# Optimization experiments

Hardware: AMD Instinct MI355X
Metric: run time of the kernel (lower is better)

## Reference

```python
import jax, jax.numpy as jnp
import numpy as np

DIM = 192
HRES, WRES = 64, 64
NUM_HEADS = 6
WS = 8  # window_size
MLP_HIDDEN = int(DIM * 4.0)
EPS = 1e-5


def layer_norm(x, gamma, beta):
    mu = jnp.mean(x, axis=-1, keepdims=True)
    var = jnp.var(x, axis=-1, keepdims=True)
    return (x - mu) * jax.lax.rsqrt(var + EPS) * gamma + beta


def window_partition(x, ws):
    B, H, W, C = x.shape
    x = x.reshape(B, H // ws, ws, W // ws, ws, C)
    x = jnp.transpose(x, (0, 1, 3, 2, 4, 5))
    return x.reshape(-1, ws * ws, C)


def window_reverse(windows, ws, H, W, C):
    B = windows.shape[0] // ((H // ws) * (W // ws))
    x = windows.reshape(B, H // ws, W // ws, ws, ws, C)
    x = jnp.transpose(x, (0, 1, 3, 2, 4, 5))
    return x.reshape(B, H, W, C)


def setup_inputs() -> dict:
    key = jax.random.key(0)
    ks = jax.random.split(key, 12)
    s = 0.02
    return {
        "x": jax.random.normal(ks[0], (32, HRES * WRES, DIM), dtype=jnp.float32),
        "norm1_g": jnp.ones((DIM,), jnp.float32),
        "norm1_b": jnp.zeros((DIM,), jnp.float32),
        "qkv_w": jax.random.normal(ks[1], (DIM, 3 * DIM), jnp.float32) * s,
        "qkv_b": jnp.zeros((3 * DIM,), jnp.float32),
        "proj_w": jax.random.normal(ks[2], (DIM, DIM), jnp.float32) * s,
        "proj_b": jnp.zeros((DIM,), jnp.float32),
        "norm2_g": jnp.ones((DIM,), jnp.float32),
        "norm2_b": jnp.zeros((DIM,), jnp.float32),
        "fc1_w": jax.random.normal(ks[3], (DIM, MLP_HIDDEN), jnp.float32) * s,
        "fc1_b": jnp.zeros((MLP_HIDDEN,), jnp.float32),
        "fc2_w": jax.random.normal(ks[4], (MLP_HIDDEN, DIM), jnp.float32) * s,
        "fc2_b": jnp.zeros((DIM,), jnp.float32),
    }


def reference(x, norm1_g, norm1_b, qkv_w, qkv_b, proj_w, proj_b,
              norm2_g, norm2_b, fc1_w, fc1_b, fc2_w, fc2_b):
    B, L, C = x.shape
    H, W = HRES, WRES
    hd = C // NUM_HEADS
    scale = hd ** -0.5

    shortcut = x
    h = layer_norm(x, norm1_g, norm1_b).reshape(B, H, W, C)
    win = window_partition(h, WS)  # [nW*B, WS*WS, C]
    Bw, N, _ = win.shape

    qkv = (win @ qkv_w + qkv_b).reshape(Bw, N, 3, NUM_HEADS, hd)
    q, k, v = jnp.transpose(qkv, (2, 0, 3, 1, 4))  # each [Bw, H, N, hd]
    attn = jnp.einsum('bhnd,bhmd->bhnm', q, k) * scale
    attn = jax.nn.softmax(attn, axis=-1)
    out = jnp.einsum('bhnm,bhmd->bhnd', attn, v)
    out = jnp.transpose(out, (0, 2, 1, 3)).reshape(Bw, N, C)
    out = out @ proj_w + proj_b

    h = window_reverse(out, WS, H, W, C).reshape(B, L, C)
    x = shortcut + h

    m = layer_norm(x, norm2_g, norm2_b)
    m = jax.nn.gelu(m @ fc1_w + fc1_b, approximate=False)
    m = m @ fc2_w + fc2_b
    return x + m
```

## Files before the change

kernel.cpp:

```cpp
#include <hip/hip_runtime.h>
#include <hip/hip_bf16.h>
#include <math.h>

#define DIM   192
#define NH    6
#define HD    32
#define WSZ   8
#define HRES_ 64
#define WRES_ 64
#define BATCH 32
#define LTOK  (HRES_*WRES_)
#define MTOK  (BATCH*LTOK)
#define QKVN  (3*DIM)
#define MLPH  (4*DIM)

using bf16 = __hip_bfloat16;
using bf16x8 = __attribute__((ext_vector_type(8))) short;
using f32x4  = __attribute__((ext_vector_type(4))) float;

__device__ __forceinline__ float bf2f(bf16 h) { return __bfloat162float(h); }
__device__ __forceinline__ float us2f(unsigned short u) {
    union { unsigned u32; float f; } c; c.u32 = ((unsigned)u) << 16; return c.f;
}


__global__ void detect_kernel(const unsigned short* __restrict__ g, int* __restrict__ flag)
{
    *flag = (g[0] == 0x3F80) ? 0 : 1;
}

__global__ __launch_bounds__(256) void cvt_kernel(
    const void* __restrict__ src, bf16* __restrict__ dst,
    long n, long elem_off, const int* __restrict__ flag)
{
    long i = ((long)blockIdx.x * 256 + threadIdx.x) * 8;
    if (i >= n) return;
    if (i + 8 <= n) {
        if (*flag) {
            const float* s = (const float*)src + elem_off + i;
            float4 a = *reinterpret_cast<const float4*>(s);
            float4 b = *reinterpret_cast<const float4*>(s + 4);
            bf16 o[8];
            o[0]=__float2bfloat16(a.x); o[1]=__float2bfloat16(a.y);
            o[2]=__float2bfloat16(a.z); o[3]=__float2bfloat16(a.w);
            o[4]=__float2bfloat16(b.x); o[5]=__float2bfloat16(b.y);
            o[6]=__float2bfloat16(b.z); o[7]=__float2bfloat16(b.w);
            *reinterpret_cast<bf16x8*>(dst + i) = *reinterpret_cast<const bf16x8*>(o);
        } else {
            *reinterpret_cast<bf16x8*>(dst + i) =
                *reinterpret_cast<const bf16x8*>((const bf16*)src + elem_off + i);
        }
    } else {
        for (long k2 = i; k2 < n; ++k2) {
            if (*flag) dst[k2] = __float2bfloat16(((const float*)src)[elem_off + k2]);
            else       dst[k2] = ((const bf16*)src)[elem_off + k2];
        }
    }
}

__global__ __launch_bounds__(256) void ln1_fused(
    const void* __restrict__ x, long eoff, const int* __restrict__ flag,
    const bf16* __restrict__ g, const bf16* __restrict__ b, bf16* __restrict__ y)
{
    int wave = threadIdx.x >> 6;
    int lane = threadIdx.x & 63;
    long token = (long)blockIdx.x * 4 + wave;
    int fl = *flag;
    float f0, f1, f2;
    if (fl) {
        const float* xp = (const float*)x + eoff + token * DIM;
        f0 = xp[lane]; f1 = xp[lane + 64]; f2 = xp[lane + 128];
    } else {
        const bf16* xp = (const bf16*)x + eoff + token * DIM;
        f0 = bf2f(xp[lane]); f1 = bf2f(xp[lane + 64]); f2 = bf2f(xp[lane + 128]);
    }
    float s  = f0 + f1 + f2;
    float ss = f0*f0 + f1*f1 + f2*f2;
    #pragma unroll
    for (int m = 1; m < 64; m <<= 1) { s += __shfl_xor(s, m); ss += __shfl_xor(ss, m); }
    float mean = s * (1.0f/192.0f);
    float var  = ss * (1.0f/192.0f) - mean*mean;
    float rstd = rsqrtf(var + 1e-5f);
    bf16* yp = y + token * DIM;
    yp[lane]       = __float2bfloat16((f0-mean)*rstd*bf2f(g[lane])       + bf2f(b[lane]));
    yp[lane + 64]  = __float2bfloat16((f1-mean)*rstd*bf2f(g[lane + 64])  + bf2f(b[lane + 64]));
    yp[lane + 128] = __float2bfloat16((f2-mean)*rstd*bf2f(g[lane + 128]) + bf2f(b[lane + 128]));
}

__global__ void transpose_kernel(const bf16* __restrict__ in, bf16* __restrict__ out,
                                 int K, int N)
{
    int idx = blockIdx.x * 256 + threadIdx.x;
    if (idx < K * N) {
        int n = idx % N, k = idx / N;
        out[n * K + k] = in[idx];
    }
}

template<int EPI>
__global__ __launch_bounds__(256) void gemm_bt(
    const bf16* __restrict__ A, const bf16* __restrict__ Bt,
    const bf16* __restrict__ bias, const void* __restrict__ res,
    long resoff, const int* __restrict__ flag,
    bf16* __restrict__ C, int M, int N, int K)
{
    constexpr int KC = 192;
    __shared__ __align__(16) bf16 bsh[(KC/32) * 4 * 64 * 8];
    int tid  = threadIdx.x;
    int wave = tid >> 6, lane = tid & 63;
    int t = lane & 15, q = lane >> 4;
    int  n0 = blockIdx.x * 64;
    long m0 = (long)blockIdx.y * 128;

    int fl = (EPI == 2) ? *flag : 0;
    f32x4 acc[2][4] = {};

    for (int kc = 0; kc < K; kc += KC) {
        __syncthreads();
        for (int s = tid; s < (KC/32) * 256; s += 256) {
            int ks  = s >> 8;
            int rem = s & 255;
            int j   = rem >> 6;
            int ln  = rem & 63;
            int tt = ln & 15, qq = ln >> 4;
            int n = j * 16 + tt;
            int k = ks * 32 + qq * 8;
            const float4* src = reinterpret_cast<const float4*>(
                Bt + (long)(n0 + n) * K + kc + k);
            reinterpret_cast<float4*>(bsh)[s] = *src;
        }
        __syncthreads();

        const bf16* arow = A + (m0 + wave * 32 + t) * (long)K + kc + q * 8;
        #pragma unroll
        for (int ks = 0; ks < KC/32; ++ks) {
            bf16x8 a0 = *reinterpret_cast<const bf16x8*>(arow + ks * 32);
            bf16x8 a1 = *reinterpret_cast<const bf16x8*>(arow + 16 * (long)K + ks * 32);
            #pragma unroll
            for (int j = 0; j < 4; ++j) {
                bf16x8 b = reinterpret_cast<const bf16x8*>(bsh)[ks * 256 + j * 64 + lane];
                acc[0][j] = __builtin_amdgcn_mfma_f32_16x16x32_bf16(a0, b, acc[0][j], 0, 0, 0);
                acc[1][j] = __builtin_amdgcn_mfma_f32_16x16x32_bf16(a1, b, acc[1][j], 0, 0, 0);
            }
        }
    }

    #pragma unroll
    for (int j = 0; j < 4; ++j) {
        int col = n0 + j * 16 + t;
        float bv = bf2f(bias[col]);
        #pragma unroll
        for (int i = 0; i < 2; ++i) {
            #pragma unroll
            for (int r = 0; r < 4; ++r) {
                long row = m0 + wave * 32 + i * 16 + q * 4 + r;
                float v = acc[i][j][r] + bv;
                if (EPI == 2) {
                    long ri = resoff + row * (long)N + col;
                    v += fl ? ((const float*)res)[ri]
                            : bf2f(((const bf16*)res)[ri]);
                }
                C[row * N + col] = __float2bfloat16(v);
            }
        }
    }
}

__global__ __launch_bounds__(256, 3) void mlp_kernel(
    const bf16* __restrict__ Y,   const bf16* __restrict__ W1t,
    const bf16* __restrict__ b1,  const bf16* __restrict__ W2t,
    const bf16* __restrict__ b2,  const bf16* __restrict__ n2g,
    const bf16* __restrict__ n2b, const int* __restrict__ flag,
    void* __restrict__ out, long outoff, int M)
{
    constexpr int HS = 88;
    __shared__ __align__(16) bf16 bsh[1536 * 8];
    __shared__ __align__(16) bf16 hsh[64 * HS];
    int tid  = threadIdx.x;
    int wave = tid >> 6, lane = tid & 63;
    int t = lane & 15, q = lane >> 4;
    long m0 = (long)blockIdx.x * 64;
    int fl = *flag;

    bf16x8 a_reg[6];
    {
        const bf16* yp = Y + (m0 + wave * 16 + t) * (long)DIM + q * 8;
        float s = 0.f, ss = 0.f;
        #pragma unroll
        for (int ks = 0; ks < 6; ++ks) {
            a_reg[ks] = *reinterpret_cast<const bf16x8*>(yp + ks * 32);
            #pragma unroll
            for (int e = 0; e < 8; ++e) {
                float f = us2f((unsigned short)a_reg[ks][e]);
                s += f; ss += f * f;
            }
        }
        s  += __shfl_xor(s, 16);  s  += __shfl_xor(s, 32);
        ss += __shfl_xor(ss, 16); ss += __shfl_xor(ss, 32);
        float mean = s * (1.0f/192.0f);
        float var  = ss * (1.0f/192.0f) - mean * mean;
        float rstd = rsqrtf(var + 1e-5f);
        #pragma unroll
        for (int ks = 0; ks < 6; ++ks) {
            bf16x8 gk = *reinterpret_cast<const bf16x8*>(n2g + ks * 32 + q * 8);
            bf16x8 bk = *reinterpret_cast<const bf16x8*>(n2b + ks * 32 + q * 8);
            bf16 tmp[8];
            #pragma unroll
            for (int e = 0; e < 8; ++e) {
                float f = us2f((unsigned short)a_reg[ks][e]);
                float v = (f - mean) * rstd * us2f((unsigned short)gk[e])
                          + us2f((unsigned short)bk[e]);
                tmp[e] = __float2bfloat16(v);
            }
            a_reg[ks] = *reinterpret_cast<const bf16x8*>(tmp);
        }
    }

    f32x4 oacc[12] = {};

    for (int nc = 0; nc < 12; ++nc) {
        __syncthreads();
        #pragma unroll
        for (int it = 0; it < 6; ++it) {
            int s   = it * 256 + tid;
            int ks  = s >> 8;
            int rem = s & 255;
            int j   = rem >> 6;
            int ln  = rem & 63;
            int n   = nc * 64 + j * 16 + (ln & 15);
            int k   = ks * 32 + (ln >> 4) * 8;
            reinterpret_cast<float4*>(bsh)[s] =
                *reinterpret_cast<const float4*>(W1t + (long)n * DIM + k);
        }
        __syncthreads();

        f32x4 hacc[4] = {};
        #pragma unroll
        for (int ks = 0; ks < 6; ++ks) {
            #pragma unroll
            for (int j = 0; j < 4; ++j) {
                bf16x8 b = reinterpret_cast<const bf16x8*>(bsh)[ks * 256 + j * 64 + lane];
                hacc[j] = __builtin_amdgcn_mfma_f32_16x16x32_bf16(a_reg[ks], b, hacc[j], 0, 0, 0);
            }
        }
        #pragma unroll
        for (int j = 0; j < 4; ++j) {
            float bv = bf2f(b1[nc * 64 + j * 16 + t]);
            #pragma unroll
            for (int r = 0; r < 4; ++r) {
                int row = wave * 16 + q * 4 + r;
                float v = hacc[j][r] + bv;
                v = v * 0.5f * (1.0f + erff(v * 0.70710678118f));
                hsh[row * HS + j * 16 + t] = __float2bfloat16(v);
            }
        }
        __syncthreads();

        #pragma unroll
        for (int it = 0; it < 6; ++it) {
            int s   = it * 256 + tid;
            int ks  = s / 768;
            int rem = s - ks * 768;
            int j   = rem >> 6;
            int ln  = rem & 63;
            int n   = j * 16 + (ln & 15);
            int k   = nc * 64 + ks * 32 + (ln >> 4) * 8;
            reinterpret_cast<float4*>(bsh)[s] =
                *reinterpret_cast<const float4*>(W2t + (long)n * MLPH + k);
        }
        __syncthreads();

        #pragma unroll
        for (int ks = 0; ks < 2; ++ks) {
            bf16x8 h = *reinterpret_cast<const bf16x8*>(hsh + (wave * 16 + t) * HS + ks * 32 + q * 8);
            #pragma unroll
            for (int j = 0; j < 12; ++j) {
                bf16x8 b = reinterpret_cast<const bf16x8*>(bsh)[ks * 768 + j * 64 + lane];
                oacc[j] = __builtin_amdgcn_mfma_f32_16x16x32_bf16(h, b, oacc[j], 0, 0, 0);
            }
        }
    }

    #pragma unroll
    for (int j = 0; j < 12; ++j) {
        int col = j * 16 + t;
        float bv = bf2f(b2[col]);
        #pragma unroll
        for (int r = 0; r < 4; ++r) {
            long row = m0 + wave * 16 + q * 4 + r;
            float v = oacc[j][r] + bv + bf2f(Y[row * DIM + col]);
            long oi = outoff + row * DIM + col;
            if (fl) ((float*)out)[oi] = v;
            else    ((bf16*)out)[oi]  = __float2bfloat16(v);
        }
    }
}

__global__ __launch_bounds__(256) void attn_kernel(
    const bf16* __restrict__ qkv, bf16* __restrict__ out)
{
    int win  = blockIdx.x;
    int head = blockIdx.y;
    __shared__ __align__(16) bf16 qs[64 * 32];
    __shared__ __align__(16) bf16 ksm[64 * 32];
    __shared__ __align__(16) bf16 vt[32 * 64];
    __shared__ __align__(16) bf16 ps[64 * 64];
    __shared__ int nat[64];

    int tid  = threadIdx.x;
    int wave = tid >> 6, lane = tid & 63;
    int t = lane & 15, q = lane >> 4;

    if (tid < 64) {
        int b = win >> 6;
        int widx = win & 63;
        int wh = widx >> 3, ww = widx & 7;
        int r = wh * 8 + (tid >> 3);
        int c = ww * 8 + (tid & 7);
        nat[tid] = b * LTOK + r * WRES_ + c;
    }
    __syncthreads();

    {
        int token = tid >> 2, ch = tid & 3;
        long base = (long)nat[token] * QKVN + head * HD + ch * 8;
        float4 qv = *reinterpret_cast<const float4*>(qkv + base);
        float4 kv = *reinterpret_cast<const float4*>(qkv + base + DIM);
        float4 vv = *reinterpret_cast<const float4*>(qkv + base + 2 * DIM);
        *reinterpret_cast<float4*>(qs  + token * 32 + ch * 8) = qv;
        *reinterpret_cast<float4*>(ksm + token * 32 + ch * 8) = kv;
        const bf16* vp = reinterpret_cast<const bf16*>(&vv);
        #pragma unroll
        for (int e = 0; e < 8; ++e) vt[(ch * 8 + e) * 64 + token] = vp[e];
    }
    __syncthreads();

    f32x4 sacc[4] = {};
    {
        bf16x8 aq = *reinterpret_cast<const bf16x8*>(qs + (wave * 16 + t) * 32 + q * 8);
        #pragma unroll
        for (int j = 0; j < 4; ++j) {
            bf16x8 bk = *reinterpret_cast<const bf16x8*>(ksm + (j * 16 + t) * 32 + q * 8);
            sacc[j] = __builtin_amdgcn_mfma_f32_16x16x32_bf16(aq, bk, sacc[j], 0, 0, 0);
        }
    }

    const float scale = 0.17677669529663689f;
    #pragma unroll
    for (int r = 0; r < 4; ++r) {
        float m_ = fmaxf(fmaxf(sacc[0][r], sacc[1][r]), fmaxf(sacc[2][r], sacc[3][r]));
        #pragma unroll
        for (int msk = 1; msk < 16; msk <<= 1) m_ = fmaxf(m_, __shfl_xor(m_, msk));
        float p[4], sum = 0.f;
        #pragma unroll
        for (int j = 0; j < 4; ++j) { p[j] = expf((sacc[j][r] - m_) * scale); sum += p[j]; }
        #pragma unroll
        for (int msk = 1; msk < 16; msk <<= 1) sum += __shfl_xor(sum, msk);
        float inv = 1.0f / sum;
        int row = wave * 16 + q * 4 + r;
        #pragma unroll
        for (int j = 0; j < 4; ++j)
            ps[row * 64 + j * 16 + t] = __float2bfloat16(p[j] * inv);
    }
    __syncthreads();

    f32x4 oacc[2] = {};
    #pragma unroll
    for (int kk = 0; kk < 2; ++kk) {
        bf16x8 ap = *reinterpret_cast<const bf16x8*>(ps + (wave * 16 + t) * 64 + kk * 32 + q * 8);
        #pragma unroll
        for (int j = 0; j < 2; ++j) {
            bf16x8 bv = *reinterpret_cast<const bf16x8*>(vt + (j * 16 + t) * 64 + kk * 32 + q * 8);
            oacc[j] = __builtin_amdgcn_mfma_f32_16x16x32_bf16(ap, bv, oacc[j], 0, 0, 0);
        }
    }
    #pragma unroll
    for (int j = 0; j < 2; ++j) {
        #pragma unroll
        for (int r = 0; r < 4; ++r) {
            int row = wave * 16 + q * 4 + r;
            out[(long)nat[row] * DIM + head * HD + j * 16 + t] = __float2bfloat16(oacc[j][r]);
        }
    }
}

extern "C" void kernel_launch(void* const* d_in, const int* in_sizes, int n_in,
                              void* d_out, int out_size, void* d_ws, size_t ws_size,
                              hipStream_t stream)
{
    char* ws = (char*)d_ws;
    size_t off = 0;
    auto alloc = [&](size_t bytes) {
        char* p = ws + off;
        off += (bytes + 255) & ~(size_t)255;
        return p;
    };

    int* flag = (int*)alloc(sizeof(int));

    static const int psz[12] = { DIM, DIM, DIM*QKVN, QKVN, DIM*DIM, DIM,
                                 DIM, DIM, DIM*MLPH, MLPH, MLPH*DIM, DIM };
    bf16* par[12];
    for (int i = 0; i < 12; ++i) par[i] = (bf16*)alloc((size_t)psz[i] * 2);
    bf16 *n1g = par[0], *n1b = par[1], *qkvw = par[2], *qkvb = par[3],
         *projw = par[4], *projb = par[5], *n2g = par[6], *n2b = par[7],
         *fc1w = par[8], *fc1b = par[9], *fc2w = par[10], *fc2b = par[11];

    bf16* wqkv_t  = (bf16*)alloc((size_t)QKVN * DIM * 2);
    bf16* wproj_t = (bf16*)alloc((size_t)DIM * DIM * 2);
    bf16* wfc1_t  = (bf16*)alloc((size_t)MLPH * DIM * 2);
    bf16* wfc2_t  = (bf16*)alloc((size_t)DIM * MLPH * 2);
    size_t fixed_off = off;

    int C = 32;
    while (C > 1) {
        size_t Mc = (size_t)C * LTOK;
        if (fixed_off + Mc * 1920 + 4096 <= ws_size) break;
        C >>= 1;
    }
    size_t Mc = (size_t)C * LTOK;
    bf16* R  = (bf16*)alloc(Mc * 384);
    bf16* Y  = (bf16*)alloc(Mc * 384);
    bf16* S  = (bf16*)alloc(Mc * 1152);
    int nchunks = BATCH / C;

    detect_kernel<<<1, 1, 0, stream>>>((const unsigned short*)d_in[1], flag);

    for (int i = 0; i < 12; ++i) {
        unsigned blocks = (unsigned)(((long)psz[i] + 8*256 - 1) / (8*256));
        cvt_kernel<<<blocks, 256, 0, stream>>>(d_in[i + 1], par[i], psz[i], 0, flag);
    }

    transpose_kernel<<<(DIM*QKVN + 255)/256, 256, 0, stream>>>(qkvw, wqkv_t, DIM, QKVN);
    transpose_kernel<<<(DIM*DIM  + 255)/256, 256, 0, stream>>>(projw, wproj_t, DIM, DIM);
    transpose_kernel<<<(DIM*MLPH + 255)/256, 256, 0, stream>>>(fc1w, wfc1_t, DIM, MLPH);
    transpose_kernel<<<(MLPH*DIM + 255)/256, 256, 0, stream>>>(fc2w, wfc2_t, MLPH, DIM);

    for (int ci = 0; ci < nchunks; ++ci) {
        long eoff = (long)ci * Mc * DIM;

        ln1_fused<<<(unsigned)(Mc/4), 256, 0, stream>>>(d_in[0], eoff, flag, n1g, n1b, R);
        gemm_bt<0><<<dim3(QKVN/64, Mc/128), 256, 0, stream>>>(R, wqkv_t, qkvb, nullptr, 0, flag, S, (int)Mc, QKVN, DIM);
        attn_kernel<<<dim3(C*64, NH), 256, 0, stream>>>(S, R);
        gemm_bt<2><<<dim3(DIM/64, Mc/128), 256, 0, stream>>>(R, wproj_t, projb, d_in[0], eoff, flag, Y, (int)Mc, DIM, DIM);
        mlp_kernel<<<(unsigned)(Mc/64), 256, 0, stream>>>(Y, wfc1_t, fc1b, wfc2_t, fc2b, n2g, n2b, flag, d_out, eoff, (int)Mc);
    }
}
```

Before: 705.3 us.

## Fuse QKV projection GEMM into windowed attention kernel

Replaces the separate QKV GEMM plus attention kernel with one kernel that computes each window-head's Q, K, V slices directly from the normalized activations via MFMA and writes them into shared memory. This removes the write and re-read of the large QKV intermediate buffer and one launch. It also shrinks workspace needs, which may allow larger chunks. In exchange, each window's LN output rows are re-read once per head (six times), weight tiles are fetched from global or cache per block, and occupancy is bounded by launch_bounds 4.

```diff
diff --git a/kernel.cpp b/kernel.cpp
--- a/kernel.cpp
+++ b/kernel.cpp
@@ -166,6 +166,119 @@
     }
 }
 
+__global__ __launch_bounds__(256, 4) void qkv_attn_kernel(
+    const bf16* __restrict__ R, const bf16* __restrict__ Wt,
+    const bf16* __restrict__ qkvb, bf16* __restrict__ out)
+{
+    int win  = blockIdx.x;
+    int head = blockIdx.y;
+    __shared__ __align__(16) bf16 qs[64 * 32];
+    __shared__ __align__(16) bf16 ksm[64 * 32];
+    __shared__ __align__(16) bf16 vt[32 * 64];
+    __shared__ __align__(16) bf16 ps[64 * 64];
+    __shared__ int nat[64];
+
+    int tid  = threadIdx.x;
+    int wave = tid >> 6, lane = tid & 63;
+    int t = lane & 15, q = lane >> 4;
+
+    if (tid < 64) {
+        int b = win >> 6;
+        int widx = win & 63;
+        int wh = widx >> 3, ww = widx & 7;
+        int r = wh * 8 + (tid >> 3);
+        int c = ww * 8 + (tid & 7);
+        nat[tid] = b * LTOK + r * WRES_ + c;
+    }
+    __syncthreads();
+
+    {
+        bf16x8 a_reg[6];
+        long arow = (long)nat[wave * 16 + t] * DIM;
+        #pragma unroll
+        for (int ks = 0; ks < 6; ++ks)
+            a_reg[ks] = *reinterpret_cast<const bf16x8*>(R + arow + ks * 32 + q * 8);
+
+        f32x4 qacc[2] = {}, kacc[2] = {}, vacc[2] = {};
+        #pragma unroll
+        for (int ks = 0; ks < 6; ++ks) {
+            #pragma unroll
+            for (int j = 0; j < 2; ++j) {
+                int nq = head * HD + j * 16 + t;
+                bf16x8 bq = *reinterpret_cast<const bf16x8*>(Wt + (long)nq * DIM + ks * 32 + q * 8);
+                bf16x8 bk = *reinterpret_cast<const bf16x8*>(Wt + (long)(nq + DIM) * DIM + ks * 32 + q * 8);
+                bf16x8 bv = *reinterpret_cast<const bf16x8*>(Wt + (long)(nq + 2 * DIM) * DIM + ks * 32 + q * 8);
+                qacc[j] = __builtin_amdgcn_mfma_f32_16x16x32_bf16(a_reg[ks], bq, qacc[j], 0, 0, 0);
+                kacc[j] = __builtin_amdgcn_mfma_f32_16x16x32_bf16(a_reg[ks], bk, kacc[j], 0, 0, 0);
+                vacc[j] = __builtin_amdgcn_mfma_f32_16x16x32_bf16(a_reg[ks], bv, vacc[j], 0, 0, 0);
+            }
+        }
+        #pragma unroll
+        for (int j = 0; j < 2; ++j) {
+            int col = j * 16 + t;
+            float bq = bf2f(qkvb[head * HD + col]);
+            float bk = bf2f(qkvb[DIM + head * HD + col]);
+            float bv = bf2f(qkvb[2 * DIM + head * HD + col]);
+            #pragma unroll
+            for (int r = 0; r < 4; ++r) {
+                int row = wave * 16 + q * 4 + r;
+                qs [row * 32 + col] = __float2bfloat16(qacc[j][r] + bq);
+                ksm[row * 32 + col] = __float2bfloat16(kacc[j][r] + bk);
+                vt [col * 64 + row] = __float2bfloat16(vacc[j][r] + bv);
+            }
+        }
+    }
+    __syncthreads();
+
+    f32x4 sacc[4] = {};
+    {
+        bf16x8 aq = *reinterpret_cast<const bf16x8*>(qs + (wave * 16 + t) * 32 + q * 8);
+        #pragma unroll
+        for (int j = 0; j < 4; ++j) {
+            bf16x8 bk = *reinterpret_cast<const bf16x8*>(ksm + (j * 16 + t) * 32 + q * 8);
+            sacc[j] = __builtin_amdgcn_mfma_f32_16x16x32_bf16(aq, bk, sacc[j], 0, 0, 0);
+        }
+    }
+
+    const float scale = 0.17677669529663689f;
+    #pragma unroll
+    for (int r = 0; r < 4; ++r) {
+        float m_ = fmaxf(fmaxf(sacc[0][r], sacc[1][r]), fmaxf(sacc[2][r], sacc[3][r]));
+        #pragma unroll
+        for (int msk = 1; msk < 16; msk <<= 1) m_ = fmaxf(m_, __shfl_xor(m_, msk));
+        float p[4], sum = 0.f;
+        #pragma unroll
+        for (int j = 0; j < 4; ++j) { p[j] = expf((sacc[j][r] - m_) * scale); sum += p[j]; }
+        #pragma unroll
+        for (int msk = 1; msk < 16; msk <<= 1) sum += __shfl_xor(sum, msk);
+        float inv = 1.0f / sum;
+        int row = wave * 16 + q * 4 + r;
+        #pragma unroll
+        for (int j = 0; j < 4; ++j)
+            ps[row * 64 + j * 16 + t] = __float2bfloat16(p[j] * inv);
+    }
+    __syncthreads();
+
+    f32x4 oacc[2] = {};
+    #pragma unroll
+    for (int kk = 0; kk < 2; ++kk) {
+        bf16x8 ap = *reinterpret_cast<const bf16x8*>(ps + (wave * 16 + t) * 64 + kk * 32 + q * 8);
+        #pragma unroll
+        for (int j = 0; j < 2; ++j) {
+            bf16x8 bv = *reinterpret_cast<const bf16x8*>(vt + (j * 16 + t) * 64 + kk * 32 + q * 8);
+            oacc[j] = __builtin_amdgcn_mfma_f32_16x16x32_bf16(ap, bv, oacc[j], 0, 0, 0);
+        }
+    }
+    #pragma unroll
+    for (int j = 0; j < 2; ++j) {
+        #pragma unroll
+        for (int r = 0; r < 4; ++r) {
+            int row = wave * 16 + q * 4 + r;
+            out[(long)nat[row] * DIM + head * HD + j * 16 + t] = __float2bfloat16(oacc[j][r]);
+        }
+    }
+}
+
 __global__ __launch_bounds__(256, 3) void mlp_kernel(
     const bf16* __restrict__ Y,   const bf16* __restrict__ W1t,
     const bf16* __restrict__ b1,  const bf16* __restrict__ W2t,
@@ -296,94 +409,6 @@
     }
 }
 
-__global__ __launch_bounds__(256) void attn_kernel(
-    const bf16* __restrict__ qkv, bf16* __restrict__ out)
-{
-    int win  = blockIdx.x;
-    int head = blockIdx.y;
-    __shared__ __align__(16) bf16 qs[64 * 32];
-    __shared__ __align__(16) bf16 ksm[64 * 32];
-    __shared__ __align__(16) bf16 vt[32 * 64];
-    __shared__ __align__(16) bf16 ps[64 * 64];
-    __shared__ int nat[64];
-
-    int tid  = threadIdx.x;
-    int wave = tid >> 6, lane = tid & 63;
-    int t = lane & 15, q = lane >> 4;
-
-    if (tid < 64) {
-        int b = win >> 6;
-        int widx = win & 63;
-        int wh = widx >> 3, ww = widx & 7;
-        int r = wh * 8 + (tid >> 3);
-        int c = ww * 8 + (tid & 7);
-        nat[tid] = b * LTOK + r * WRES_ + c;
-    }
-    __syncthreads();
-
-    {
-        int token = tid >> 2, ch = tid & 3;
-        long base = (long)nat[token] * QKVN + head * HD + ch * 8;
-        float4 qv = *reinterpret_cast<const float4*>(qkv + base);
-        float4 kv = *reinterpret_cast<const float4*>(qkv + base + DIM);
-        float4 vv = *reinterpret_cast<const float4*>(qkv + base + 2 * DIM);
-        *reinterpret_cast<float4*>(qs  + token * 32 + ch * 8) = qv;
-        *reinterpret_cast<float4*>(ksm + token * 32 + ch * 8) = kv;
-        const bf16* vp = reinterpret_cast<const bf16*>(&vv);
-        #pragma unroll
-        for (int e = 0; e < 8; ++e) vt[(ch * 8 + e) * 64 + token] = vp[e];
-    }
-    __syncthreads();
-
-    f32x4 sacc[4] = {};
-    {
-        bf16x8 aq = *reinterpret_cast<const bf16x8*>(qs + (wave * 16 + t) * 32 + q * 8);
-        #pragma unroll
-        for (int j = 0; j < 4; ++j) {
-            bf16x8 bk = *reinterpret_cast<const bf16x8*>(ksm + (j * 16 + t) * 32 + q * 8);
-            sacc[j] = __builtin_amdgcn_mfma_f32_16x16x32_bf16(aq, bk, sacc[j], 0, 0, 0);
-        }
-    }
-
-    const float scale = 0.17677669529663689f;
-    #pragma unroll
-    for (int r = 0; r < 4; ++r) {
-        float m_ = fmaxf(fmaxf(sacc[0][r], sacc[1][r]), fmaxf(sacc[2][r], sacc[3][r]));
-        #pragma unroll
-        for (int msk = 1; msk < 16; msk <<= 1) m_ = fmaxf(m_, __shfl_xor(m_, msk));
-        float p[4], sum = 0.f;
-        #pragma unroll
-        for (int j = 0; j < 4; ++j) { p[j] = expf((sacc[j][r] - m_) * scale); sum += p[j]; }
-        #pragma unroll
-        for (int msk = 1; msk < 16; msk <<= 1) sum += __shfl_xor(sum, msk);
-        float inv = 1.0f / sum;
-        int row = wave * 16 + q * 4 + r;
-        #pragma unroll
-        for (int j = 0; j < 4; ++j)
-            ps[row * 64 + j * 16 + t] = __float2bfloat16(p[j] * inv);
-    }
-    __syncthreads();
-
-    f32x4 oacc[2] = {};
-    #pragma unroll
-    for (int kk = 0; kk < 2; ++kk) {
-        bf16x8 ap = *reinterpret_cast<const bf16x8*>(ps + (wave * 16 + t) * 64 + kk * 32 + q * 8);
-        #pragma unroll
-        for (int j = 0; j < 2; ++j) {
-            bf16x8 bv = *reinterpret_cast<const bf16x8*>(vt + (j * 16 + t) * 64 + kk * 32 + q * 8);
-            oacc[j] = __builtin_amdgcn_mfma_f32_16x16x32_bf16(ap, bv, oacc[j], 0, 0, 0);
-        }
-    }
-    #pragma unroll
-    for (int j = 0; j < 2; ++j) {
-        #pragma unroll
-        for (int r = 0; r < 4; ++r) {
-            int row = wave * 16 + q * 4 + r;
-            out[(long)nat[row] * DIM + head * HD + j * 16 + t] = __float2bfloat16(oacc[j][r]);
-        }
-    }
-}
-
 extern "C" void kernel_launch(void* const* d_in, const int* in_sizes, int n_in,
                               void* d_out, int out_size, void* d_ws, size_t ws_size,
                               hipStream_t stream)
@@ -415,13 +440,13 @@
     int C = 32;
     while (C > 1) {
         size_t Mc = (size_t)C * LTOK;
-        if (fixed_off + Mc * 1920 + 4096 <= ws_size) break;
+        if (fixed_off + Mc * 1152 + 4096 <= ws_size) break;
         C >>= 1;
     }
     size_t Mc = (size_t)C * LTOK;
     bf16* R  = (bf16*)alloc(Mc * 384);
+    bf16* T  = (bf16*)alloc(Mc * 384);
     bf16* Y  = (bf16*)alloc(Mc * 384);
-    bf16* S  = (bf16*)alloc(Mc * 1152);
     int nchunks = BATCH / C;
 
     detect_kernel<<<1, 1, 0, stream>>>((const unsigned short*)d_in[1], flag);
@@ -440,9 +465,8 @@
         long eoff = (long)ci * Mc * DIM;
 
         ln1_fused<<<(unsigned)(Mc/4), 256, 0, stream>>>(d_in[0], eoff, flag, n1g, n1b, R);
-        gemm_bt<0><<<dim3(QKVN/64, Mc/128), 256, 0, stream>>>(R, wqkv_t, qkvb, nullptr, 0, flag, S, (int)Mc, QKVN, DIM);
-        attn_kernel<<<dim3(C*64, NH), 256, 0, stream>>>(S, R);
-        gemm_bt<2><<<dim3(DIM/64, Mc/128), 256, 0, stream>>>(R, wproj_t, projb, d_in[0], eoff, flag, Y, (int)Mc, DIM, DIM);
+        qkv_attn_kernel<<<dim3(C*64, NH), 256, 0, stream>>>(R, wqkv_t, qkvb, T);
+        gemm_bt<2><<<dim3(DIM/64, Mc/128), 256, 0, stream>>>(T, wproj_t, projb, d_in[0], eoff, flag, Y, (int)Mc, DIM, DIM);
         mlp_kernel<<<(unsigned)(Mc/64), 256, 0, stream>>>(Y, wfc1_t, fc1b, wfc2_t, fc2b, n2g, n2b, flag, d_out, eoff, (int)Mc);
     }
 }
```

New measurement: 757.0 us. 1.07x slower.
